# Performance work log

Measured on AMD Instinct MI355X. Metric: run time of the kernel, lower is better.

The kernel has to match this reference:

```python
import jax, jax.numpy as jnp
import numpy as np

D_MODEL = 1024
N_HEADS = 16
D_K = D_MODEL // N_HEADS  # 64
D_FF = int(8 * D_MODEL / 3)  # 2730
THETA = 10000.0
MAX_SEQ_LEN = 2048
BATCH = 2
SEQ = 2048
EPS = 1e-5


def setup_inputs() -> dict:
    key = jax.random.key(0)
    ks = jax.random.split(key, 10)

    def lin(k, d_out, d_in):
        sigma = np.sqrt(2.0 / (d_out + d_in))
        w = jax.random.truncated_normal(k, -3.0, 3.0, (d_out, d_in), dtype=jnp.float32)
        return w * sigma

    x = jax.random.normal(ks[0], (BATCH, SEQ, D_MODEL), dtype=jnp.float32)
    token_positions = jnp.tile(jnp.arange(SEQ, dtype=jnp.int32)[None, :], (BATCH, 1))
    return {
        "x": x,
        "token_positions": token_positions,
        "WQ": lin(ks[1], D_MODEL, D_MODEL),
        "WK": lin(ks[2], D_MODEL, D_MODEL),
        "WV": lin(ks[3], D_MODEL, D_MODEL),
        "WO": lin(ks[4], D_MODEL, D_MODEL),
        "W1": lin(ks[5], D_FF, D_MODEL),
        "W2": lin(ks[6], D_MODEL, D_FF),
        "W3": lin(ks[7], D_FF, D_MODEL),
        "g1": jnp.ones((D_MODEL,), dtype=jnp.float32),
        "g2": jnp.ones((D_MODEL,), dtype=jnp.float32),
    }


def _rmsnorm(x, g):
    xf = x.astype(jnp.float32)
    inv = jax.lax.rsqrt(jnp.mean(xf * xf, axis=-1, keepdims=True) + EPS)
    return (xf * inv * g).astype(x.dtype)


def _rope(x, pos):
    # x: [b, h, t, d_k]; pos: [b, t] int. Pairs are consecutive (x0,x1).
    half = D_K // 2
    inv_freq = THETA ** (-(2.0 * jnp.arange(1, half + 1, dtype=jnp.float32) - 2.0) / D_K)
    ang = pos.astype(jnp.float32)[..., None] * inv_freq  # [b, t, half]
    cos = jnp.cos(ang)[:, None, :, :]  # [b, 1, t, half]
    sin = jnp.sin(ang)[:, None, :, :]
    xr = x.reshape(*x.shape[:-1], half, 2)
    x0, x1 = xr[..., 0], xr[..., 1]
    out = jnp.stack([cos * x0 - sin * x1, sin * x0 + cos * x1], axis=-1)
    return out.reshape(x.shape)


def reference(x, token_positions, WQ, WK, WV, WO, W1, W2, W3, g1, g2):
    b, t, _ = x.shape
    # --- attention sublayer (pre-norm) ---
    h = _rmsnorm(x, g1)
    q = jnp.einsum('btd,ed->bte', h, WQ).reshape(b, t, N_HEADS, D_K).transpose(0, 2, 1, 3)
    k = jnp.einsum('btd,ed->bte', h, WK).reshape(b, t, N_HEADS, D_K).transpose(0, 2, 1, 3)
    v = jnp.einsum('btd,ed->bte', h, WV).reshape(b, t, N_HEADS, D_K).transpose(0, 2, 1, 3)
    q = _rope(q, token_positions)
    k = _rope(k, token_positions)
    scores = jnp.einsum('bhqd,bhkd->bhqk', q, k) * (D_K ** -0.5)
    causal = jnp.tril(jnp.ones((t, t), dtype=bool))
    scores = jnp.where(causal, scores, -jnp.inf)
    attn = jax.nn.softmax(scores, axis=-1)
    o = jnp.einsum('bhqk,bhkd->bhqd', attn, v)
    o = o.transpose(0, 2, 1, 3).reshape(b, t, D_MODEL)
    o = jnp.einsum('btd,ed->bte', o, WO)
    x = x + o
    # --- SwiGLU FFN sublayer (pre-norm) ---
    h = _rmsnorm(x, g2)
    u = jnp.einsum('btd,fd->btf', h, W1)
    g = jnp.einsum('btd,fd->btf', h, W3)
    ff = jnp.einsum('btf,df->btd', (u * jax.nn.sigmoid(u)) * g, W2)
    return x + ff
```

## Files before the change

kernel.cpp:

```cpp
#include <hip/hip_runtime.h>
#include <cstdint>

#define BT_ROWS 4096
#define DM      1024
#define DFF     2730
#define DFFP    2816
#define TSEQ    2048

typedef float  f32x4  __attribute__((ext_vector_type(4)));
typedef __bf16 bf16x8 __attribute__((ext_vector_type(8)));

typedef __attribute__((address_space(1))) const unsigned int as1_uint;
typedef __attribute__((address_space(3))) unsigned int       as3_uint;

__device__ __forceinline__ unsigned short f2bf(float f) {
  union { float f; unsigned int u; } v; v.f = f;
  unsigned int u = v.u;
  return (unsigned short)((u + 0x7fffu + ((u >> 16) & 1u)) >> 16);
}
__device__ __forceinline__ float bf2f(unsigned int b) {
  union { unsigned int u; float f; } v; v.u = b << 16;
  return v.f;
}

__device__ __forceinline__ void async_cp16(const void* g, void* l) {
  __builtin_amdgcn_global_load_lds((as1_uint*)(uintptr_t)g, (as3_uint*)(uintptr_t)l, 16, 0, 0);
}

__global__ void prep_kernel(const float* __restrict__ WQ, const float* __restrict__ WK,
                            const float* __restrict__ WV, const float* __restrict__ WOp,
                            const float* __restrict__ W1, const float* __restrict__ W3,
                            const float* __restrict__ W2, const int* __restrict__ pos,
                            unsigned short* __restrict__ Wqkv, unsigned short* __restrict__ Wo,
                            unsigned short* __restrict__ W13i, unsigned short* __restrict__ W2p,
                            float* __restrict__ ct, float* __restrict__ st) {
  long idx = (long)blockIdx.x * 256 + threadIdx.x;
  if (idx < 4194304) {
    const int j = (int)(idx >> 20);
    const long t = idx & 1048575;
    const float* s = (j == 0) ? WQ : (j == 1) ? WK : (j == 2) ? WV : WOp;
    unsigned short* d = (j < 3) ? (Wqkv + (size_t)j * 1048576) : Wo;
    d[t] = f2bf(s[t]);
    return;
  }
  idx -= 4194304;
  if (idx < 2L * DFFP * 1024) {
    const int half = (int)(idx / (DFFP * 1024));
    const long t = idx % (DFFP * 1024);
    const int r = (int)(t >> 10), c = (int)(t & 1023);
    const float v = (r < DFF) ? (half ? W3 : W1)[(long)r * 1024 + c] : 0.f;
    W13i[((long)2 * r + half) * 1024 + c] = f2bf(v);
    return;
  }
  idx -= 2L * DFFP * 1024;
  if (idx < 1024L * DFFP) {
    const int c = (int)(idx % DFFP), r = (int)(idx / DFFP);
    const float v = (c < DFF) ? W2[(long)r * DFF + c] : 0.f;
    W2p[idx] = f2bf(v);
    return;
  }
  idx -= 1024L * DFFP;
  if (idx < BT_ROWS * 32) {
    const int r = (int)(idx >> 5), i = (int)(idx & 31);
    const float f = powf(10000.f, -(float)(2 * i) * (1.f / 64.f));
    float sv, cv;
    sincosf((float)pos[r] * f, &sv, &cv);
    ct[idx] = cv; st[idx] = sv;
  }
}
#define PREP_TOTAL (4194304L + 2L * DFFP * 1024 + 1024L * DFFP + BT_ROWS * 32)

__global__ void rmsnorm_kernel(const float* __restrict__ x, const float* __restrict__ g,
                               unsigned short* __restrict__ out) {
  const int row = blockIdx.x, tid = threadIdx.x;
  const float4 xv = reinterpret_cast<const float4*>(x + (long)row * DM)[tid];
  float ss = xv.x * xv.x + xv.y * xv.y + xv.z * xv.z + xv.w * xv.w;
#pragma unroll
  for (int o = 32; o > 0; o >>= 1) ss += __shfl_xor(ss, o);
  __shared__ float wsum[4];
  if ((tid & 63) == 0) wsum[tid >> 6] = ss;
  __syncthreads();
  const float inv = rsqrtf((wsum[0] + wsum[1] + wsum[2] + wsum[3]) * (1.f / DM) + 1e-5f);
  const float4 gv = reinterpret_cast<const float4*>(g)[tid];
  ushort4 o4;
  o4.x = f2bf(xv.x * inv * gv.x);
  o4.y = f2bf(xv.y * inv * gv.y);
  o4.z = f2bf(xv.z * inv * gv.z);
  o4.w = f2bf(xv.w * inv * gv.w);
  reinterpret_cast<ushort4*>(out + (long)row * DM)[tid] = o4;
}

__global__ void rope_kernel(unsigned short* __restrict__ QK,
                            const float* __restrict__ ct, const float* __restrict__ st) {
  int idx = blockIdx.x * 256 + threadIdx.x;
  if (idx >= BT_ROWS * 512) return;
  int r = idx >> 9, p = idx & 511;
  int h = p >> 5, i = p & 31;
  float c = ct[r * 32 + i], s = st[r * 32 + i];
  unsigned int* base = reinterpret_cast<unsigned int*>(QK + (long)r * 2048 + h * 64 + 2 * i);
  unsigned int q01 = base[0];
  float x0 = bf2f(q01 & 0xffffu), x1 = bf2f(q01 >> 16);
  base[0] = (unsigned int)f2bf(c * x0 - s * x1) | ((unsigned int)f2bf(s * x0 + c * x1) << 16);
  unsigned int k01 = base[512];
  float y0 = bf2f(k01 & 0xffffu), y1 = bf2f(k01 >> 16);
  base[512] = (unsigned int)f2bf(c * y0 - s * y1) | ((unsigned int)f2bf(s * y0 + c * y1) << 16);
}

template <int EPI, int BN>
__global__ __launch_bounds__(256) void gemm_bt(
    const unsigned short* __restrict__ A, const unsigned short* __restrict__ B,
    void* __restrict__ C, const float* __restrict__ resid,
    int M, int N, int K, int ldc) {
  constexpr int WNF = BN / 32;
  __shared__ unsigned short As[2][128 * 64];
  __shared__ unsigned short Bs[2][BN * 64];
  const int tid = threadIdx.x;
  const int wid = tid >> 6;
  const int lane = tid & 63;
  const long rowBase = (long)blockIdx.y * 128;
  const long colBase = (long)blockIdx.x * BN;
  const int wm = (wid >> 1) * 64;
  const int wn = (wid & 1) * (BN / 2);
  const int srow = wid * 8 + (lane >> 3);
  const int sc   = lane & 7;
  const int cs   = (sc ^ (srow & 7)) * 8;
  const int fr = lane & 15;
  const int fg = lane >> 4;

  const f32x4 z4 = {0.f, 0.f, 0.f, 0.f};
  f32x4 acc[4][WNF];
#pragma unroll
  for (int m = 0; m < 4; ++m)
#pragma unroll
    for (int n = 0; n < WNF; ++n) acc[m][n] = z4;

  auto stage = [&](int buf, int kt) {
    const long kOff = (long)kt * 64 + cs;
    char* AsB = (char*)As[buf];
    char* BsB = (char*)Bs[buf];
#pragma unroll
    for (int i = 0; i < 4; ++i)
      async_cp16(A + (rowBase + i * 32 + srow) * K + kOff, AsB + i * 4096 + wid * 1024);
#pragma unroll
    for (int i = 0; i < WNF; ++i)
      async_cp16(B + (colBase + i * 32 + srow) * K + kOff, BsB + i * 4096 + wid * 1024);
  };

  const int nkt = K >> 6;
  stage(0, 0);
  __syncthreads();
  for (int kt = 0; kt < nkt; ++kt) {
    if (kt + 1 < nkt) stage((kt + 1) & 1, kt + 1);
    const char* AsB = (const char*)As[kt & 1];
    const char* BsB = (const char*)Bs[kt & 1];
#pragma unroll
    for (int kk = 0; kk < 2; ++kk) {
      bf16x8 af[4], bfr[WNF];
#pragma unroll
      for (int m = 0; m < 4; ++m)
        af[m] = *(const bf16x8*)(AsB + (wm + m * 16 + fr) * 128 + (((kk * 4 + fg) ^ (fr & 7)) * 16));
#pragma unroll
      for (int n = 0; n < WNF; ++n)
        bfr[n] = *(const bf16x8*)(BsB + (wn + n * 16 + fr) * 128 + (((kk * 4 + fg) ^ (fr & 7)) * 16));
#pragma unroll
      for (int m = 0; m < 4; ++m)
#pragma unroll
        for (int n = 0; n < WNF; ++n)
          acc[m][n] = __builtin_amdgcn_mfma_f32_16x16x32_bf16(af[m], bfr[n], acc[m][n], 0, 0, 0);
    }
    __syncthreads();
  }

  const int erow = fg * 4;
  if (EPI == 0) {
    unsigned short* Cp = (unsigned short*)C;
#pragma unroll
    for (int m = 0; m < 4; ++m) {
      const long r0 = rowBase + wm + m * 16 + erow;
#pragma unroll
      for (int n = 0; n < WNF; ++n) {
        const long col = colBase + wn + n * 16 + fr;
#pragma unroll
        for (int r = 0; r < 4; ++r) Cp[(r0 + r) * ldc + col] = f2bf(acc[m][n][r]);
      }
    }
  } else if (EPI == 1) {
    float* Cf = (float*)C;
#pragma unroll
    for (int m = 0; m < 4; ++m) {
      const long r0 = rowBase + wm + m * 16 + erow;
#pragma unroll
      for (int n = 0; n < WNF; ++n) {
        const long col = colBase + wn + n * 16 + fr;
#pragma unroll
        for (int r = 0; r < 4; ++r) {
          const long o = (r0 + r) * ldc + col;
          Cf[o] = acc[m][n][r] + resid[o];
        }
      }
    }
  } else {
    unsigned short* Cp = (unsigned short*)C;
    const int even = !(fr & 1);
#pragma unroll
    for (int m = 0; m < 4; ++m) {
      const long r0 = rowBase + wm + m * 16 + erow;
#pragma unroll
      for (int n = 0; n < WNF; ++n) {
        const long col = colBase + wn + n * 16 + fr;
        const long fcol = col >> 1;
#pragma unroll
        for (int r = 0; r < 4; ++r) {
          const float own = acc[m][n][r];
          const float oth = __shfl_xor(own, 1);
          if (even) {
            const float s = own * oth / (1.f + __expf(-own));
            Cp[(r0 + r) * ldc + fcol] = f2bf(s);
          }
        }
      }
    }
  }
}

#define KSTR 72
__global__ __launch_bounds__(256) void attn_kernel(
    const unsigned short* __restrict__ QK, const unsigned short* __restrict__ Vt,
    unsigned short* __restrict__ O) {
  __shared__ unsigned short Ks[2][64 * KSTR];
  const int bh = blockIdx.x;
  const int b = bh >> 4, h = bh & 15;
  const int tid = threadIdx.x;
  const int wid = tid >> 6, lane = tid & 63;
  const int qblk = 31 - blockIdx.y;
  const int qbase = qblk * 64 + wid * 16;
  const int fr = lane & 15, g = lane >> 4;
  const long rowb = (long)b * TSEQ;
  const int hoff = h * 64;
  const float C2 = 0.18033688011112042f;

  const int ki = tid >> 3;
  const int kcol = (tid & 7) * 8;
  const int kgrow = 8 * ((ki & 15) >> 2) + (ki & 3) + ((ki >> 4) << 2);

  const unsigned short* qrow = QK + (rowb + qbase + fr) * 2048 + hoff + g * 8;
  const bf16x8 qb0 = *reinterpret_cast<const bf16x8*>(qrow);
  const bf16x8 qb1 = *reinterpret_cast<const bf16x8*>(qrow + 32);

  const unsigned short* Kg = QK + rowb * 2048 + 1024 + hoff;
  const unsigned short* Vrow = Vt + (long)(hoff + fr) * 4096 + rowb + g * 8;

  const f32x4 z4 = {0.f, 0.f, 0.f, 0.f};
  f32x4 acc[4];
#pragma unroll
  for (int d = 0; d < 4; ++d) acc[d] = z4;
  float mrun = -1e30f, lrun = 0.f;
  const int qg = qbase + fr;
  const int nkt = qblk + 1;

  uint4 kr0 = *reinterpret_cast<const uint4*>(Kg + (long)kgrow * 2048 + kcol);
  uint4 kr1 = *reinterpret_cast<const uint4*>(Kg + (long)(32 + kgrow) * 2048 + kcol);

  for (int kt = 0; kt < nkt; ++kt) {
    unsigned short* Kb = Ks[kt & 1];
    *reinterpret_cast<uint4*>(&Kb[ki * KSTR + kcol]) = kr0;
    *reinterpret_cast<uint4*>(&Kb[(32 + ki) * KSTR + kcol]) = kr1;
    __syncthreads();
    const int kbase = kt * 64;
    if (kt + 1 < nkt) {
      kr0 = *reinterpret_cast<const uint4*>(Kg + (long)(kbase + 64 + kgrow) * 2048 + kcol);
      kr1 = *reinterpret_cast<const uint4*>(Kg + (long)(kbase + 96 + kgrow) * 2048 + kcol);
    }
    bf16x8 vf[4][2];
#pragma unroll
    for (int db = 0; db < 4; ++db)
#pragma unroll
      for (int ks = 0; ks < 2; ++ks)
        vf[db][ks] = *reinterpret_cast<const bf16x8*>(Vrow + (size_t)db * 16 * 4096 + kbase + ks * 32);

    f32x4 s1[2], s2[2];
#pragma unroll
    for (int ks = 0; ks < 2; ++ks) {
      const unsigned short* ra = &Kb[(ks * 32 + fr) * KSTR];
      const unsigned short* rc = &Kb[(ks * 32 + 16 + fr) * KSTR];
      f32x4 t1 = z4, t2 = z4;
      t1 = __builtin_amdgcn_mfma_f32_16x16x32_bf16(*reinterpret_cast<const bf16x8*>(ra + g * 8), qb0, t1, 0, 0, 0);
      t1 = __builtin_amdgcn_mfma_f32_16x16x32_bf16(*reinterpret_cast<const bf16x8*>(ra + 32 + g * 8), qb1, t1, 0, 0, 0);
      t2 = __builtin_amdgcn_mfma_f32_16x16x32_bf16(*reinterpret_cast<const bf16x8*>(rc + g * 8), qb0, t2, 0, 0, 0);
      t2 = __builtin_amdgcn_mfma_f32_16x16x32_bf16(*reinterpret_cast<const bf16x8*>(rc + 32 + g * 8), qb1, t2, 0, 0, 0);
      s1[ks] = t1; s2[ks] = t2;
    }

    float sc[16];
    if (kt + 1 < nkt) {
#pragma unroll
      for (int ks = 0; ks < 2; ++ks)
#pragma unroll
        for (int j = 0; j < 4; ++j) {
          sc[ks * 8 + j] = s1[ks][j];
          sc[ks * 8 + 4 + j] = s2[ks][j];
        }
    } else {
      const int kb8 = kbase + 8 * g;
#pragma unroll
      for (int ks = 0; ks < 2; ++ks)
#pragma unroll
        for (int j = 0; j < 4; ++j) {
          sc[ks * 8 + j]     = (kb8 + ks * 32 + j     <= qg) ? s1[ks][j] : -1e30f;
          sc[ks * 8 + 4 + j] = (kb8 + ks * 32 + 4 + j <= qg) ? s2[ks][j] : -1e30f;
        }
    }
    const float t0 = fmaxf(fmaxf(sc[0], sc[1]), sc[2]);
    const float t1 = fmaxf(fmaxf(sc[3], sc[4]), sc[5]);
    const float t2 = fmaxf(fmaxf(sc[6], sc[7]), sc[8]);
    const float t3 = fmaxf(fmaxf(sc[9], sc[10]), sc[11]);
    const float t4 = fmaxf(fmaxf(sc[12], sc[13]), sc[14]);
    float tmax = fmaxf(fmaxf(fmaxf(t0, t1), t2), fmaxf(fmaxf(t3, t4), sc[15]));
    tmax = fmaxf(tmax, __shfl_xor(tmax, 16));
    tmax = fmaxf(tmax, __shfl_xor(tmax, 32));
    if (__any(tmax > mrun)) {
      const float mnew = fmaxf(mrun, tmax);
      const float alpha = exp2f((mrun - mnew) * C2);
#pragma unroll
      for (int db = 0; db < 4; ++db)
#pragma unroll
        for (int r = 0; r < 4; ++r) acc[db][r] *= alpha;
      lrun *= alpha;
      mrun = mnew;
    }
    const float m2 = mrun * C2;
    bf16x8 pbv[2];
    float psum = 0.f;
#pragma unroll
    for (int ks = 0; ks < 2; ++ks)
#pragma unroll
      for (int j = 0; j < 8; ++j) {
        const float p = exp2f(fmaf(sc[ks * 8 + j], C2, -m2));
        psum += p;
        pbv[ks][j] = (__bf16)p;
      }
    psum += __shfl_xor(psum, 16);
    psum += __shfl_xor(psum, 32);
    lrun += psum;

#pragma unroll
    for (int db = 0; db < 4; ++db) {
      acc[db] = __builtin_amdgcn_mfma_f32_16x16x32_bf16(vf[db][0], pbv[0], acc[db], 0, 0, 0);
      acc[db] = __builtin_amdgcn_mfma_f32_16x16x32_bf16(vf[db][1], pbv[1], acc[db], 0, 0, 0);
    }
  }

  const float inv = 1.f / lrun;
  unsigned short* orow = O + (rowb + qbase + fr) * DM + hoff;
#pragma unroll
  for (int db = 0; db < 4; ++db) {
    uint2 pk;
    pk.x = (unsigned int)f2bf(acc[db][0] * inv) | ((unsigned int)f2bf(acc[db][1] * inv) << 16);
    pk.y = (unsigned int)f2bf(acc[db][2] * inv) | ((unsigned int)f2bf(acc[db][3] * inv) << 16);
    *reinterpret_cast<uint2*>(orow + db * 16 + g * 4) = pk;
  }
}

static constexpr size_t OFF_WQKV = 0;
static constexpr size_t OFF_WO   = 6291456;
static constexpr size_t OFF_W13  = 8388608;
static constexpr size_t OFF_W2   = 19922944;
static constexpr size_t OFF_H    = 25690112;
static constexpr size_t OFF_X2   = 34078720;
static constexpr size_t OFF_CT   = 50855936;
static constexpr size_t OFF_ST   = 51380224;
static constexpr size_t OFF_QK   = 51904512;
static constexpr size_t OFF_VT   = 68681728;
static constexpr size_t OFF_HO   = 77070336;

extern "C" void kernel_launch(void* const* d_in, const int* in_sizes, int n_in,
                              void* d_out, int out_size, void* d_ws, size_t ws_size,
                              hipStream_t stream) {
  const float* x  = (const float*)d_in[0];
  const int* tpos = (const int*)d_in[1];
  const float* WQ = (const float*)d_in[2];
  const float* WK = (const float*)d_in[3];
  const float* WV = (const float*)d_in[4];
  const float* WO = (const float*)d_in[5];
  const float* W1 = (const float*)d_in[6];
  const float* W2 = (const float*)d_in[7];
  const float* W3 = (const float*)d_in[8];
  const float* g1 = (const float*)d_in[9];
  const float* g2 = (const float*)d_in[10];
  float* out = (float*)d_out;

  char* ws = (char*)d_ws;
  unsigned short* Wqkv = (unsigned short*)(ws + OFF_WQKV);
  unsigned short* Wo   = (unsigned short*)(ws + OFF_WO);
  unsigned short* W13i = (unsigned short*)(ws + OFF_W13);
  unsigned short* W2p  = (unsigned short*)(ws + OFF_W2);
  unsigned short* hbuf = (unsigned short*)(ws + OFF_H);
  float* x2            = (float*)(ws + OFF_X2);
  float* ct            = (float*)(ws + OFF_CT);
  float* st            = (float*)(ws + OFF_ST);
  unsigned short* QKb  = (unsigned short*)(ws + OFF_QK);
  unsigned short* Sbuf = (unsigned short*)(ws + OFF_QK);
  unsigned short* Vtb  = (unsigned short*)(ws + OFF_VT);
  unsigned short* Ho   = (unsigned short*)(ws + OFF_HO);

  prep_kernel<<<(int)((PREP_TOTAL + 255) / 256), 256, 0, stream>>>(
      WQ, WK, WV, WO, W1, W3, W2, tpos, Wqkv, Wo, W13i, W2p, ct, st);

  rmsnorm_kernel<<<BT_ROWS, 256, 0, stream>>>(x, g1, hbuf);
  gemm_bt<0, 128><<<dim3(16, 32), 256, 0, stream>>>(hbuf, Wqkv, QKb, nullptr, BT_ROWS, 2048, 1024, 2048);
  gemm_bt<0, 64><<<dim3(64, 8), 256, 0, stream>>>(Wqkv + 2048 * 1024, hbuf, Vtb, nullptr, 1024, BT_ROWS, 1024, BT_ROWS);
  rope_kernel<<<(BT_ROWS * 512) / 256, 256, 0, stream>>>(QKb, ct, st);
  attn_kernel<<<dim3(32, 32), 256, 0, stream>>>(QKb, Vtb, Ho);
  gemm_bt<1, 64><<<dim3(16, 32), 256, 0, stream>>>(Ho, Wo, x2, x, BT_ROWS, 1024, 1024, 1024);

  rmsnorm_kernel<<<BT_ROWS, 256, 0, stream>>>(x2, g2, hbuf);
  gemm_bt<3, 128><<<dim3(44, 32), 256, 0, stream>>>(hbuf, W13i, Sbuf, nullptr, BT_ROWS, 2 * DFFP, 1024, DFFP);
  gemm_bt<1, 64><<<dim3(16, 32), 256, 0, stream>>>(Sbuf, W2p, out, x2, BT_ROWS, 1024, DFFP, 1024);
}
```

Measured before the change: 274.6 us.

## Fuse RoPE into QK GEMM epilogue and load K directly into registers in attention

Removes the separate rope kernel by applying the rotation in a new GEMM epilogue (EPI 4) using interleaved cos/sin pairs stored as float2. The attention kernel drops its LDS double-buffered K tile and __syncthreads, and instead loads K fragments straight from global memory into MFMA operands each iteration. This saves a kernel launch plus a read-modify-write pass over Q/K, and removes block-level syncs. The cost is that K loads are no longer prefetched a tile ahead or shared through LDS across waves, so memory latency may be more exposed.

```diff
diff --git a/kernel.cpp b/kernel.cpp
--- a/kernel.cpp
+++ b/kernel.cpp
@@ -33,7 +33,7 @@
                             const float* __restrict__ W2, const int* __restrict__ pos,
                             unsigned short* __restrict__ Wqkv, unsigned short* __restrict__ Wo,
                             unsigned short* __restrict__ W13i, unsigned short* __restrict__ W2p,
-                            float* __restrict__ ct, float* __restrict__ st) {
+                            float2* __restrict__ cs) {
   long idx = (long)blockIdx.x * 256 + threadIdx.x;
   if (idx < 4194304) {
     const int j = (int)(idx >> 20);
@@ -65,7 +65,7 @@
     const float f = powf(10000.f, -(float)(2 * i) * (1.f / 64.f));
     float sv, cv;
     sincosf((float)pos[r] * f, &sv, &cv);
-    ct[idx] = cv; st[idx] = sv;
+    cs[idx] = make_float2(cv, sv);
   }
 }
 #define PREP_TOTAL (4194304L + 2L * DFFP * 1024 + 1024L * DFFP + BT_ROWS * 32)
@@ -90,26 +90,11 @@
   reinterpret_cast<ushort4*>(out + (long)row * DM)[tid] = o4;
 }
 
-__global__ void rope_kernel(unsigned short* __restrict__ QK,
-                            const float* __restrict__ ct, const float* __restrict__ st) {
-  int idx = blockIdx.x * 256 + threadIdx.x;
-  if (idx >= BT_ROWS * 512) return;
-  int r = idx >> 9, p = idx & 511;
-  int h = p >> 5, i = p & 31;
-  float c = ct[r * 32 + i], s = st[r * 32 + i];
-  unsigned int* base = reinterpret_cast<unsigned int*>(QK + (long)r * 2048 + h * 64 + 2 * i);
-  unsigned int q01 = base[0];
-  float x0 = bf2f(q01 & 0xffffu), x1 = bf2f(q01 >> 16);
-  base[0] = (unsigned int)f2bf(c * x0 - s * x1) | ((unsigned int)f2bf(s * x0 + c * x1) << 16);
-  unsigned int k01 = base[512];
-  float y0 = bf2f(k01 & 0xffffu), y1 = bf2f(k01 >> 16);
-  base[512] = (unsigned int)f2bf(c * y0 - s * y1) | ((unsigned int)f2bf(s * y0 + c * y1) << 16);
-}
-
 template <int EPI, int BN>
 __global__ __launch_bounds__(256) void gemm_bt(
     const unsigned short* __restrict__ A, const unsigned short* __restrict__ B,
     void* __restrict__ C, const float* __restrict__ resid,
+    const float2* __restrict__ CS,
     int M, int N, int K, int ldc) {
   constexpr int WNF = BN / 32;
   __shared__ unsigned short As[2][128 * 64];
@@ -199,7 +184,7 @@
         }
       }
     }
-  } else {
+  } else if (EPI == 3) {
     unsigned short* Cp = (unsigned short*)C;
     const int even = !(fr & 1);
 #pragma unroll
@@ -220,14 +205,32 @@
         }
       }
     }
-  }
-}
-
-#define KSTR 72
+  } else {
+    unsigned short* Cp = (unsigned short*)C;
+    const int even = !(fr & 1);
+#pragma unroll
+    for (int m = 0; m < 4; ++m) {
+      const long r0 = rowBase + wm + m * 16 + erow;
+#pragma unroll
+      for (int n = 0; n < WNF; ++n) {
+        const long col = colBase + wn + n * 16 + fr;
+        const int i = (int)((col & 63) >> 1);
+#pragma unroll
+        for (int r = 0; r < 4; ++r) {
+          const float own = acc[m][n][r];
+          const float oth = __shfl_xor(own, 1);
+          const float2 cv = CS[(r0 + r) * 32 + i];
+          const float v = even ? (cv.x * own - cv.y * oth) : (cv.y * oth + cv.x * own);
+          Cp[(r0 + r) * ldc + col] = f2bf(v);
+        }
+      }
+    }
+  }
+}
+
 __global__ __launch_bounds__(256) void attn_kernel(
     const unsigned short* __restrict__ QK, const unsigned short* __restrict__ Vt,
     unsigned short* __restrict__ O) {
-  __shared__ unsigned short Ks[2][64 * KSTR];
   const int bh = blockIdx.x;
   const int b = bh >> 4, h = bh & 15;
   const int tid = threadIdx.x;
@@ -239,15 +242,12 @@
   const int hoff = h * 64;
   const float C2 = 0.18033688011112042f;
 
-  const int ki = tid >> 3;
-  const int kcol = (tid & 7) * 8;
-  const int kgrow = 8 * ((ki & 15) >> 2) + (ki & 3) + ((ki >> 4) << 2);
-
   const unsigned short* qrow = QK + (rowb + qbase + fr) * 2048 + hoff + g * 8;
   const bf16x8 qb0 = *reinterpret_cast<const bf16x8*>(qrow);
   const bf16x8 qb1 = *reinterpret_cast<const bf16x8*>(qrow + 32);
 
   const unsigned short* Kg = QK + rowb * 2048 + 1024 + hoff;
+  const unsigned short* pK = Kg + (long)(8 * (fr >> 2) + (fr & 3)) * 2048 + g * 8;
   const unsigned short* Vrow = Vt + (long)(hoff + fr) * 4096 + rowb + g * 8;
 
   const f32x4 z4 = {0.f, 0.f, 0.f, 0.f};
@@ -258,19 +258,17 @@
   const int qg = qbase + fr;
   const int nkt = qblk + 1;
 
-  uint4 kr0 = *reinterpret_cast<const uint4*>(Kg + (long)kgrow * 2048 + kcol);
-  uint4 kr1 = *reinterpret_cast<const uint4*>(Kg + (long)(32 + kgrow) * 2048 + kcol);
-
   for (int kt = 0; kt < nkt; ++kt) {
-    unsigned short* Kb = Ks[kt & 1];
-    *reinterpret_cast<uint4*>(&Kb[ki * KSTR + kcol]) = kr0;
-    *reinterpret_cast<uint4*>(&Kb[(32 + ki) * KSTR + kcol]) = kr1;
-    __syncthreads();
     const int kbase = kt * 64;
-    if (kt + 1 < nkt) {
-      kr0 = *reinterpret_cast<const uint4*>(Kg + (long)(kbase + 64 + kgrow) * 2048 + kcol);
-      kr1 = *reinterpret_cast<const uint4*>(Kg + (long)(kbase + 96 + kgrow) * 2048 + kcol);
-    }
+    const long o = (long)kbase * 2048;
+    const bf16x8 ka0 = *(const bf16x8*)(pK + o);
+    const bf16x8 ka1 = *(const bf16x8*)(pK + o + 32);
+    const bf16x8 kb0 = *(const bf16x8*)(pK + o + 8192);
+    const bf16x8 kb1 = *(const bf16x8*)(pK + o + 8192 + 32);
+    const bf16x8 kc0 = *(const bf16x8*)(pK + o + 65536);
+    const bf16x8 kc1 = *(const bf16x8*)(pK + o + 65536 + 32);
+    const bf16x8 kd0 = *(const bf16x8*)(pK + o + 65536 + 8192);
+    const bf16x8 kd1 = *(const bf16x8*)(pK + o + 65536 + 8192 + 32);
     bf16x8 vf[4][2];
 #pragma unroll
     for (int db = 0; db < 4; ++db)
@@ -279,17 +277,14 @@
         vf[db][ks] = *reinterpret_cast<const bf16x8*>(Vrow + (size_t)db * 16 * 4096 + kbase + ks * 32);
 
     f32x4 s1[2], s2[2];
-#pragma unroll
-    for (int ks = 0; ks < 2; ++ks) {
-      const unsigned short* ra = &Kb[(ks * 32 + fr) * KSTR];
-      const unsigned short* rc = &Kb[(ks * 32 + 16 + fr) * KSTR];
-      f32x4 t1 = z4, t2 = z4;
-      t1 = __builtin_amdgcn_mfma_f32_16x16x32_bf16(*reinterpret_cast<const bf16x8*>(ra + g * 8), qb0, t1, 0, 0, 0);
-      t1 = __builtin_amdgcn_mfma_f32_16x16x32_bf16(*reinterpret_cast<const bf16x8*>(ra + 32 + g * 8), qb1, t1, 0, 0, 0);
-      t2 = __builtin_amdgcn_mfma_f32_16x16x32_bf16(*reinterpret_cast<const bf16x8*>(rc + g * 8), qb0, t2, 0, 0, 0);
-      t2 = __builtin_amdgcn_mfma_f32_16x16x32_bf16(*reinterpret_cast<const bf16x8*>(rc + 32 + g * 8), qb1, t2, 0, 0, 0);
-      s1[ks] = t1; s2[ks] = t2;
-    }
+    s1[0] = __builtin_amdgcn_mfma_f32_16x16x32_bf16(ka0, qb0, z4, 0, 0, 0);
+    s1[0] = __builtin_amdgcn_mfma_f32_16x16x32_bf16(ka1, qb1, s1[0], 0, 0, 0);
+    s2[0] = __builtin_amdgcn_mfma_f32_16x16x32_bf16(kb0, qb0, z4, 0, 0, 0);
+    s2[0] = __builtin_amdgcn_mfma_f32_16x16x32_bf16(kb1, qb1, s2[0], 0, 0, 0);
+    s1[1] = __builtin_amdgcn_mfma_f32_16x16x32_bf16(kc0, qb0, z4, 0, 0, 0);
+    s1[1] = __builtin_amdgcn_mfma_f32_16x16x32_bf16(kc1, qb1, s1[1], 0, 0, 0);
+    s2[1] = __builtin_amdgcn_mfma_f32_16x16x32_bf16(kd0, qb0, z4, 0, 0, 0);
+    s2[1] = __builtin_amdgcn_mfma_f32_16x16x32_bf16(kd1, qb1, s2[1], 0, 0, 0);
 
     float sc[16];
     if (kt + 1 < nkt) {
@@ -367,8 +362,7 @@
 static constexpr size_t OFF_W2   = 19922944;
 static constexpr size_t OFF_H    = 25690112;
 static constexpr size_t OFF_X2   = 34078720;
-static constexpr size_t OFF_CT   = 50855936;
-static constexpr size_t OFF_ST   = 51380224;
+static constexpr size_t OFF_CS   = 50855936;
 static constexpr size_t OFF_QK   = 51904512;
 static constexpr size_t OFF_VT   = 68681728;
 static constexpr size_t OFF_HO   = 77070336;
@@ -396,24 +390,22 @@
   unsigned short* W2p  = (unsigned short*)(ws + OFF_W2);
   unsigned short* hbuf = (unsigned short*)(ws + OFF_H);
   float* x2            = (float*)(ws + OFF_X2);
-  float* ct            = (float*)(ws + OFF_CT);
-  float* st            = (float*)(ws + OFF_ST);
+  float2* cs           = (float2*)(ws + OFF_CS);
   unsigned short* QKb  = (unsigned short*)(ws + OFF_QK);
   unsigned short* Sbuf = (unsigned short*)(ws + OFF_QK);
   unsigned short* Vtb  = (unsigned short*)(ws + OFF_VT);
   unsigned short* Ho   = (unsigned short*)(ws + OFF_HO);
 
   prep_kernel<<<(int)((PREP_TOTAL + 255) / 256), 256, 0, stream>>>(
-      WQ, WK, WV, WO, W1, W3, W2, tpos, Wqkv, Wo, W13i, W2p, ct, st);
+      WQ, WK, WV, WO, W1, W3, W2, tpos, Wqkv, Wo, W13i, W2p, cs);
 
   rmsnorm_kernel<<<BT_ROWS, 256, 0, stream>>>(x, g1, hbuf);
-  gemm_bt<0, 128><<<dim3(16, 32), 256, 0, stream>>>(hbuf, Wqkv, QKb, nullptr, BT_ROWS, 2048, 1024, 2048);
-  gemm_bt<0, 64><<<dim3(64, 8), 256, 0, stream>>>(Wqkv + 2048 * 1024, hbuf, Vtb, nullptr, 1024, BT_ROWS, 1024, BT_ROWS);
-  rope_kernel<<<(BT_ROWS * 512) / 256, 256, 0, stream>>>(QKb, ct, st);
+  gemm_bt<4, 128><<<dim3(16, 32), 256, 0, stream>>>(hbuf, Wqkv, QKb, nullptr, cs, BT_ROWS, 2048, 1024, 2048);
+  gemm_bt<0, 64><<<dim3(64, 8), 256, 0, stream>>>(Wqkv + 2048 * 1024, hbuf, Vtb, nullptr, nullptr, 1024, BT_ROWS, 1024, BT_ROWS);
   attn_kernel<<<dim3(32, 32), 256, 0, stream>>>(QKb, Vtb, Ho);
-  gemm_bt<1, 64><<<dim3(16, 32), 256, 0, stream>>>(Ho, Wo, x2, x, BT_ROWS, 1024, 1024, 1024);
+  gemm_bt<1, 64><<<dim3(16, 32), 256, 0, stream>>>(Ho, Wo, x2, x, nullptr, BT_ROWS, 1024, 1024, 1024);
 
   rmsnorm_kernel<<<BT_ROWS, 256, 0, stream>>>(x2, g2, hbuf);
-  gemm_bt<3, 128><<<dim3(44, 32), 256, 0, stream>>>(hbuf, W13i, Sbuf, nullptr, BT_ROWS, 2 * DFFP, 1024, DFFP);
-  gemm_bt<1, 64><<<dim3(16, 32), 256, 0, stream>>>(Sbuf, W2p, out, x2, BT_ROWS, 1024, DFFP, 1024);
-}
+  gemm_bt<3, 128><<<dim3(44, 32), 256, 0, stream>>>(hbuf, W13i, Sbuf, nullptr, nullptr, BT_ROWS, 2 * DFFP, 1024, DFFP);
+  gemm_bt<1, 64><<<dim3(16, 32), 256, 0, stream>>>(Sbuf, W2p, out, x2, nullptr, BT_ROWS, 1024, DFFP, 1024);
+}
```

Measured after the change: 339.5 us. 1.24x slower.
